# Kernel optimization log

Measured on AMD Instinct MI355X. Metric: run time of the kernel, lower is better.

The kernel has to match this reference:

```python
import jax, jax.numpy as jnp
import numpy as np

L, E, H, D, F, B, CIN, N = 12, 128, 4, 32, 512, 64, 256, 257


def setup_inputs() -> dict:
    key = jax.random.key(0)
    ks = jax.random.split(key, 10)
    s = 0.02
    rn = lambda k, shape: jax.random.normal(k, shape, jnp.float32) * s
    return {
        "feat": jax.random.normal(ks[0], (B, CIN, 32, 32), jnp.float32),
        "conv_w": rn(ks[1], (E, CIN, 3, 3)),
        "conv_b": jnp.zeros((E,), jnp.float32),
        "pos_emb": rn(ks[2], (1, N, E)),
        "cls_token": rn(ks[3], (1, 1, E)),
        "ln1_s": jnp.ones((L, E), jnp.float32),
        "ln1_b": jnp.zeros((L, E), jnp.float32),
        "qkv_w": rn(ks[4], (L, 3 * E, E)),
        "qkv_b": jnp.zeros((L, 3 * E), jnp.float32),
        "proj_w": rn(ks[5], (L, E, E)),
        "proj_b": jnp.zeros((L, E), jnp.float32),
        "ln2_s": jnp.ones((L, E), jnp.float32),
        "ln2_b": jnp.zeros((L, E), jnp.float32),
        "ffn1_w": rn(ks[6], (L, F, E)),
        "ffn1_b": jnp.zeros((L, F), jnp.float32),
        "ffn2_w": rn(ks[7], (L, E, F)),
        "ffn2_b": jnp.zeros((L, E), jnp.float32),
        "fn_s": jnp.ones((E,), jnp.float32),
        "fn_b": jnp.zeros((E,), jnp.float32),
        "fc_w": rn(ks[8], (2, E)),
        "fc_b": jnp.zeros((2,), jnp.float32),
    }


def _ln(x, s, b, eps):
    m = jnp.mean(x, -1, keepdims=True)
    v = jnp.mean((x - m) ** 2, -1, keepdims=True)
    return (x - m) * jax.lax.rsqrt(v + eps) * s + b


def reference(feat, conv_w, conv_b, pos_emb, cls_token, ln1_s, ln1_b, qkv_w,
              qkv_b, proj_w, proj_b, ln2_s, ln2_b, ffn1_w, ffn1_b, ffn2_w,
              ffn2_b, fn_s, fn_b, fc_w, fc_b):
    # patch embed: 3x3 conv stride 2 -> 16x16 = 256 tokens
    emb = jax.lax.conv_general_dilated(
        feat, conv_w, (2, 2), ((1, 1), (1, 1)),
        dimension_numbers=("NCHW", "OIHW", "NCHW")) + conv_b[None, :, None, None]
    Bsz = emb.shape[0]
    emb = emb.reshape(Bsz, E, -1).transpose(0, 2, 1)  # [B, 256, E]
    x = jnp.concatenate([jnp.broadcast_to(cls_token, (Bsz, 1, E)), emb], axis=1)
    x = x + pos_emb  # [B, N, E]
    scale = (E // H) ** -0.5

    def block(x, p):
        l1s, l1b, qw, qb, pw, pb, l2s, l2b, w1, b1, w2, b2 = p
        h = _ln(x, l1s, l1b, 1e-5)
        qkv = (h @ qw.T + qb).reshape(Bsz, N, 3, H, D).transpose(2, 0, 3, 1, 4)
        q, k, v = qkv[0], qkv[1], qkv[2]  # [B, H, N, D]
        att = jax.nn.softmax(jnp.einsum("bhnd,bhmd->bhnm", q, k) * scale, axis=-1)
        o = jnp.einsum("bhnm,bhmd->bhnd", att, v).transpose(0, 2, 1, 3).reshape(Bsz, N, E)
        x = x + (o @ pw.T + pb)
        h2 = _ln(x, l2s, l2b, 1e-5)
        x = x + (jax.nn.gelu(h2 @ w1.T + b1, approximate=False) @ w2.T + b2)
        return x, None

    x, _ = jax.lax.scan(block, x, (ln1_s, ln1_b, qkv_w, qkv_b, proj_w, proj_b,
                                   ln2_s, ln2_b, ffn1_w, ffn1_b, ffn2_w, ffn2_b))
    x = _ln(x, fn_s, fn_b, 1e-6)
    out_feat = x[:, 0, :]
    out = out_feat @ fc_w.T + fc_b
    return (out, out_feat)
```

## Files before the change

### kernel.cpp

```cpp
#include <hip/hip_runtime.h>
#include <math.h>

constexpr int NP_ = 272;
constexpr int MP_ = 64 * NP_;
constexpr int TPB_ = 17;

typedef short short8 __attribute__((ext_vector_type(8)));
typedef float f32x4 __attribute__((ext_vector_type(4)));

__device__ inline short f2bs(float f) {
    unsigned u = __builtin_bit_cast(unsigned, f);
    unsigned r = (u + 0x7fffu + ((u >> 16) & 1u)) >> 16;
    return (short)r;
}

__device__ inline f32x4 mfma16(short8 a, short8 b, f32x4 c) {
    return __builtin_amdgcn_mfma_f32_16x16x32_bf16(a, b, c, 0, 0, 0);
}

__global__ void repack_all(const float* __restrict__ qkvw, const float* __restrict__ projw,
                           const float* __restrict__ f1w, const float* __restrict__ f2w,
                           const float* __restrict__ convw,
                           short* __restrict__ wq, short* __restrict__ wp,
                           short* __restrict__ w1, short* __restrict__ w2,
                           short* __restrict__ wc) {
    int o = blockIdx.x * 256 + threadIdx.x;
    if (o < 589824) {
        int l = o / 49152, r = o % 49152;
        int chunk = r / 3072, w = r % 3072;
        int n = w >> 3, k = chunk * 8 + (w & 7);
        wq[o] = f2bs(qkvw[(size_t)l * 49152 + n * 128 + k]);
        return;
    }
    o -= 589824;
    if (o < 196608) {
        int l = o / 16384, r = o % 16384;
        int chunk = r / 1024, w = r % 1024;
        int n = w >> 3, k = chunk * 8 + (w & 7);
        wp[o] = f2bs(projw[(size_t)l * 16384 + n * 128 + k]);
        return;
    }
    o -= 196608;
    if (o < 786432) {
        int l = o / 65536, r = o % 65536;
        int chunk = r / 4096, w = r % 4096;
        int n = w >> 3, k = chunk * 8 + (w & 7);
        w1[o] = f2bs(f1w[(size_t)l * 65536 + n * 128 + k]);
        return;
    }
    o -= 786432;
    if (o < 786432) {
        int l = o / 65536, r = o % 65536;
        int chunk = r / 1024, w = r % 1024;
        int n = w >> 3, k = chunk * 8 + (w & 7);
        w2[o] = f2bs(f2w[(size_t)l * 65536 + n * 512 + k]);
        return;
    }
    o -= 786432;
    if (o < 294912) {
        int j = o & 7;
        int col = (o >> 3) & 127;
        int c = o >> 10;
        int qd = c & 3, cscb = c >> 2;
        int cs = cscb & 7, kykx = cscb >> 3;
        int cin = cs * 32 + qd * 8 + j;
        int ky = kykx / 3, kx = kykx % 3;
        wc[o] = f2bs(convw[((col * 256 + cin) * 3 + ky) * 3 + kx]);
    }
}

__global__ __launch_bounds__(256) void feat_nhwc(const float* __restrict__ feat, short* __restrict__ fp) {
    __shared__ float tile[32][33];
    int b = blockIdx.x >> 5, y = blockIdx.x & 31;
    int t = threadIdx.x;
    for (int c0 = 0; c0 < 256; c0 += 32) {
        int ci = t >> 5, x = t & 31;
        for (int cc = ci; cc < 32; cc += 8)
            tile[cc][x] = feat[((size_t)(b * 256 + c0 + cc) * 32 + y) * 32 + x];
        __syncthreads();
        for (int i = t; i < 1024; i += 256) {
            int c = i & 31, x2 = i >> 5;
            fp[((size_t)(b * 34 + y + 1) * 34 + x2 + 1) * 256 + c0 + c] = f2bs(tile[c][x2]);
        }
        __syncthreads();
    }
    short* rowp = fp + (size_t)(b * 34 + y + 1) * 34 * 256;
    for (int c = t; c < 256; c += 256) { rowp[c] = 0; rowp[33 * 256 + c] = 0; }
    if (y == 0) {
        short* r0 = fp + (size_t)(b * 34) * 34 * 256;
        for (int i = t; i < 34 * 256; i += 256) r0[i] = 0;
    }
    if (y == 31) {
        short* r33 = fp + (size_t)(b * 34 + 33) * 34 * 256;
        for (int i = t; i < 34 * 256; i += 256) r33[i] = 0;
    }
}

__global__ __launch_bounds__(256) void conv_gemm(const short* __restrict__ fp, const short* __restrict__ wr,
                                                 const float* __restrict__ cb, const float* __restrict__ pos,
                                                 const float* __restrict__ cls, float* __restrict__ X) {
    __shared__ __align__(16) short Ain[3 * 34 * 256];
    int b = blockIdx.x >> 4, oy = blockIdx.x & 15;
    int tid = threadIdx.x;
    for (int idx = tid; idx < 3 * 34 * 32; idx += 256) {
        int r = idx / 1088, rem = idx - r * 1088;
        int x = rem >> 5, c = rem & 31;
        short8 v = *(const short8*)(fp + ((size_t)(b * 34 + 2 * oy + r) * 34 + x) * 256 + c * 8);
        *(short8*)(Ain + (r * 34 + x) * 256 + ((c ^ ((x >> 1) & 7)) * 8)) = v;
    }
    __syncthreads();
    int wave = tid >> 6, lane = tid & 63;
    int ng = wave, lo = lane & 15, qd = lane >> 4;
    f32x4 acc[2] = {};
#pragma unroll
    for (int ky = 0; ky < 3; ++ky)
#pragma unroll
        for (int kx = 0; kx < 3; ++kx) {
            int sx = 2 * lo + kx;
            int arow = (ky * 34 + sx) * 256;
            int sw = (sx >> 1) & 7;
            const short* wb = wr + (((size_t)((ky * 3 + kx) * 8) * 4 + qd) * 128 + ng * 32 + lo) * 8;
#pragma unroll
            for (int cs = 0; cs < 8; ++cs) {
                short8 af = *(const short8*)(Ain + arow + (((cs * 4 + qd) ^ sw) * 8));
                short8 b0 = *(const short8*)(wb + (size_t)cs * 4096);
                short8 b1 = *(const short8*)(wb + (size_t)cs * 4096 + 128);
                acc[0] = mfma16(af, b0, acc[0]);
                acc[1] = mfma16(af, b1, acc[1]);
            }
        }
#pragma unroll
    for (int t = 0; t < 2; ++t) {
        int e = ng * 32 + t * 16 + lo;
        float bias = cb[e];
#pragma unroll
        for (int r = 0; r < 4; ++r) {
            int tok = 1 + oy * 16 + qd * 4 + r;
            X[((size_t)b * NP_ + tok) * 128 + e] = acc[t][r] + bias + pos[tok * 128 + e];
        }
    }
    if (oy == 0) {
        if (tid < 128) X[(size_t)b * NP_ * 128 + tid] = cls[tid] + pos[tid];
        for (int idx = tid; idx < 15 * 128; idx += 256)
            X[((size_t)b * NP_ + 257) * 128 + idx] = 0.f;
    }
}

__device__ inline void ln_tile16(const float* Xl, const float* __restrict__ s, const float* __restrict__ bb,
                                 short* SB, int tid, float eps) {
    int wv = tid >> 6, lane = tid & 63;
    int r4 = lane & 3, c32 = lane >> 2;
    int row = wv * 4 + r4;
    const float* xr = Xl + row * 132 + c32 * 8;
    float4 a = *(const float4*)(xr);
    float4 b = *(const float4*)(xr + 4);
    float v[8] = {a.x, a.y, a.z, a.w, b.x, b.y, b.z, b.w};
    float sum = v[0] + v[1] + v[2] + v[3] + v[4] + v[5] + v[6] + v[7];
    sum += __shfl_xor(sum, 4); sum += __shfl_xor(sum, 8);
    sum += __shfl_xor(sum, 16); sum += __shfl_xor(sum, 32);
    float mean = sum * (1.f / 128.f);
    float vs = 0.f;
#pragma unroll
    for (int j = 0; j < 8; ++j) { float d = v[j] - mean; vs += d * d; }
    vs += __shfl_xor(vs, 4); vs += __shfl_xor(vs, 8);
    vs += __shfl_xor(vs, 16); vs += __shfl_xor(vs, 32);
    float rs = rsqrtf(vs * (1.f / 128.f) + eps);
    float4 s0 = *(const float4*)(s + c32 * 8), s1 = *(const float4*)(s + c32 * 8 + 4);
    float4 b0 = *(const float4*)(bb + c32 * 8), b1 = *(const float4*)(bb + c32 * 8 + 4);
    float sv[8] = {s0.x, s0.y, s0.z, s0.w, s1.x, s1.y, s1.z, s1.w};
    float bv[8] = {b0.x, b0.y, b0.z, b0.w, b1.x, b1.y, b1.z, b1.w};
    short8 o;
#pragma unroll
    for (int j = 0; j < 8; ++j) o[j] = f2bs((v[j] - mean) * rs * sv[j] + bv[j]);
    *(short8*)(SB + (c32 * 16 + row) * 8) = o;
}

__device__ inline void qkv_stage16(const short* SB, const short* __restrict__ wq, const float* __restrict__ qb,
                                   const short8* pre, int mg, int wv, int lo, int qd,
                                   short* __restrict__ Qf, short* __restrict__ Kf, short* __restrict__ Vt) {
    int n0 = wv * 96;
    f32x4 acc[6] = {};
#pragma unroll
    for (int ki = 0; ki < 4; ++ki) {
        int kq = ki * 4 + qd;
        short8 a = *(const short8*)(SB + (kq * 16 + lo) * 8);
#pragma unroll
        for (int t = 0; t < 6; ++t) {
            short8 bf = (ki == 0) ? pre[t]
                                  : *(const short8*)(wq + ((size_t)kq * 384 + n0 + t * 16 + lo) * 8);
            acc[t] = mfma16(a, bf, acc[t]);
        }
    }
#pragma unroll
    for (int t = 0; t < 6; ++t) {
        int n = n0 + t * 16 + lo;
        float bvv = qb[n];
        int seg = n >> 7, m = n & 127, h = m >> 5, d = m & 31;
#pragma unroll
        for (int r = 0; r < 4; ++r) {
            int row = mg * 16 + qd * 4 + r;
            int bb2 = row / NP_, q = row - bb2 * NP_;
            short val = f2bs(acc[t][r] + bvv);
            if (seg == 2)
                Vt[((size_t)(bb2 * 4 + h) * 32 + d) * NP_ + q] = val;
            else
                (seg ? Kf : Qf)[((size_t)(bb2 * 4 + h) * 4 + (d >> 3)) * (NP_ * 8) + q * 8 + (d & 7)] = val;
        }
    }
}

__global__ __launch_bounds__(256, 4) void qkv0(const float* __restrict__ X, const short* __restrict__ wq,
                                               const float* __restrict__ qb, const float* __restrict__ ls,
                                               const float* __restrict__ lb,
                                               short* __restrict__ Qf, short* __restrict__ Kf,
                                               short* __restrict__ Vt) {
    __shared__ __align__(16) float Xl[16 * 132];
    __shared__ __align__(16) short SB[2048];
    int mg = blockIdx.x, tid = threadIdx.x;
    int wv = tid >> 6, lane = tid & 63, lo = lane & 15, qd = lane >> 4;
    for (int idx = tid; idx < 512; idx += 256) {
        int tok = idx >> 5, c = idx & 31;
        *(float4*)(Xl + tok * 132 + c * 4) = *(const float4*)(X + (size_t)(mg * 16 + tok) * 128 + c * 4);
    }
    short8 preq[6];
#pragma unroll
    for (int t = 0; t < 6; ++t)
        preq[t] = *(const short8*)(wq + ((size_t)qd * 384 + wv * 96 + t * 16 + lo) * 8);
    __syncthreads();
    ln_tile16(Xl, ls, lb, SB, tid, 1e-5f);
    __syncthreads();
    qkv_stage16(SB, wq, qb, preq, mg, wv, lo, qd, Qf, Kf, Vt);
}

template <int LAST>
__global__ __launch_bounds__(256, 4) void layer_tail(
    const short* __restrict__ Of, const short* __restrict__ wp, const float* __restrict__ pb,
    const float* __restrict__ l2s, const float* __restrict__ l2b,
    const short* __restrict__ w1, const float* __restrict__ b1,
    const short* __restrict__ w2, const float* __restrict__ b2,
    float* __restrict__ X,
    const float* __restrict__ l1s, const float* __restrict__ l1b,
    const short* __restrict__ wq, const float* __restrict__ qb,
    short* __restrict__ Qf, short* __restrict__ Kf, short* __restrict__ Vt) {
    __shared__ __align__(16) short SB[2048];
    __shared__ __align__(16) float Xl[16 * 132];
    __shared__ __align__(16) short Uh[32 * 136];
    int mg = blockIdx.x, tid = threadIdx.x;
    int wv = tid >> 6, lane = tid & 63, lo = lane & 15, qd = lane >> 4;
    const short* osrc = Of + (size_t)mg * 2048;
    for (int idx = tid; idx < 256; idx += 256)
        *(short8*)(SB + idx * 8) = *(const short8*)(osrc + idx * 8);
    for (int idx = tid; idx < 512; idx += 256) {
        int tok = idx >> 5, c = idx & 31;
        *(float4*)(Xl + tok * 132 + c * 4) = *(const float4*)(X + (size_t)(mg * 16 + tok) * 128 + c * 4);
    }
    int n0 = wv * 32;
    short8 prep[8];
#pragma unroll
    for (int ki = 0; ki < 4; ++ki) {
        int kq = ki * 4 + qd;
        prep[ki * 2] = *(const short8*)(wp + ((size_t)kq * 128 + n0 + lo) * 8);
        prep[ki * 2 + 1] = *(const short8*)(wp + ((size_t)kq * 128 + n0 + 16 + lo) * 8);
    }
    __syncthreads();
    {
        f32x4 pa[2] = {};
#pragma unroll
        for (int ki = 0; ki < 4; ++ki) {
            int kq = ki * 4 + qd;
            short8 a = *(const short8*)(SB + (kq * 16 + lo) * 8);
            pa[0] = mfma16(a, prep[ki * 2], pa[0]);
            pa[1] = mfma16(a, prep[ki * 2 + 1], pa[1]);
        }
        float pb0 = pb[n0 + lo], pb1 = pb[n0 + 16 + lo];
#pragma unroll
        for (int r = 0; r < 4; ++r) {
            Xl[(qd * 4 + r) * 132 + n0 + lo] += pa[0][r] + pb0;
            Xl[(qd * 4 + r) * 132 + n0 + 16 + lo] += pa[1][r] + pb1;
        }
    }
    int n0h = wv * 64;
    short8 pre1[4];
#pragma unroll
    for (int t = 0; t < 4; ++t)
        pre1[t] = *(const short8*)(w1 + ((size_t)qd * 512 + n0h + t * 16 + lo) * 8);
    __syncthreads();
    ln_tile16(Xl, l2s, l2b, SB, tid, 1e-5f);
    __syncthreads();
    f32x4 facc[2] = {};
    {
        f32x4 fa[4] = {};
#pragma unroll
        for (int ki = 0; ki < 4; ++ki) {
            int kq = ki * 4 + qd;
            short8 a = *(const short8*)(SB + (kq * 16 + lo) * 8);
#pragma unroll
            for (int t = 0; t < 4; ++t) {
                short8 bf = (ki == 0) ? pre1[t]
                                      : *(const short8*)(w1 + ((size_t)kq * 512 + n0h + t * 16 + lo) * 8);
                fa[t] = mfma16(a, bf, fa[t]);
            }
        }
#pragma unroll
        for (int t = 0; t < 4; ++t) {
            int nl = n0h + t * 16 + lo;
            float bvv = b1[nl];
#pragma unroll
            for (int r = 0; r < 4; ++r) {
                float x = fa[t][r] + bvv;
                float u = x * (0.7978845608f + 0.0356774081f * x * x);
                x = x / (1.f + __expf(-2.f * u));
                Uh[(nl >> 3) * 136 + (qd * 4 + r) * 8 + (nl & 7)] = f2bs(x);
            }
        }
    }
    short8 pre2a = *(const short8*)(w2 + ((size_t)qd * 128 + n0 + lo) * 8);
    short8 pre2b = *(const short8*)(w2 + ((size_t)qd * 128 + n0 + 16 + lo) * 8);
    short8 pre1b[4];
#pragma unroll
    for (int t = 0; t < 4; ++t)
        pre1b[t] = *(const short8*)(w1 + ((size_t)qd * 512 + 256 + n0h + t * 16 + lo) * 8);
    __syncthreads();
#pragma unroll
    for (int ki = 0; ki < 8; ++ki) {
        int kq2 = ki * 4 + qd;
        short8 a = *(const short8*)(Uh + kq2 * 136 + lo * 8);
        short8 b0 = (ki == 0) ? pre2a : *(const short8*)(w2 + ((size_t)kq2 * 128 + n0 + lo) * 8);
        short8 b1 = (ki == 0) ? pre2b : *(const short8*)(w2 + ((size_t)kq2 * 128 + n0 + 16 + lo) * 8);
        facc[0] = mfma16(a, b0, facc[0]);
        facc[1] = mfma16(a, b1, facc[1]);
    }
    short8 pre3a = *(const short8*)(w2 + ((size_t)(32 + qd) * 128 + n0 + lo) * 8);
    short8 pre3b = *(const short8*)(w2 + ((size_t)(32 + qd) * 128 + n0 + 16 + lo) * 8);
    __syncthreads();
    {
        f32x4 fa[4] = {};
#pragma unroll
        for (int ki = 0; ki < 4; ++ki) {
            int kq = ki * 4 + qd;
            short8 a = *(const short8*)(SB + (kq * 16 + lo) * 8);
#pragma unroll
            for (int t = 0; t < 4; ++t) {
                short8 bf = (ki == 0) ? pre1b[t]
                                      : *(const short8*)(w1 + ((size_t)kq * 512 + 256 + n0h + t * 16 + lo) * 8);
                fa[t] = mfma16(a, bf, fa[t]);
            }
        }
#pragma unroll
        for (int t = 0; t < 4; ++t) {
            int nl = n0h + t * 16 + lo;
            float bvv = b1[256 + nl];
#pragma unroll
            for (int r = 0; r < 4; ++r) {
                float x = fa[t][r] + bvv;
                float u = x * (0.7978845608f + 0.0356774081f * x * x);
                x = x / (1.f + __expf(-2.f * u));
                Uh[(nl >> 3) * 136 + (qd * 4 + r) * 8 + (nl & 7)] = f2bs(x);
            }
        }
    }
    __syncthreads();
#pragma unroll
    for (int ki = 0; ki < 8; ++ki) {
        int kq2 = ki * 4 + qd;
        short8 a = *(const short8*)(Uh + kq2 * 136 + lo * 8);
        short8 b0 = (ki == 0) ? pre3a : *(const short8*)(w2 + ((size_t)(32 + kq2) * 128 + n0 + lo) * 8);
        short8 b1 = (ki == 0) ? pre3b : *(const short8*)(w2 + ((size_t)(32 + kq2) * 128 + n0 + 16 + lo) * 8);
        facc[0] = mfma16(a, b0, facc[0]);
        facc[1] = mfma16(a, b1, facc[1]);
    }
    {
        float b20 = b2[n0 + lo], b21 = b2[n0 + 16 + lo];
#pragma unroll
        for (int r = 0; r < 4; ++r) {
            Xl[(qd * 4 + r) * 132 + n0 + lo] += facc[0][r] + b20;
            Xl[(qd * 4 + r) * 132 + n0 + 16 + lo] += facc[1][r] + b21;
        }
    }
    short8 preq[6];
    if (!LAST) {
#pragma unroll
        for (int t = 0; t < 6; ++t)
            preq[t] = *(const short8*)(wq + ((size_t)qd * 384 + wv * 96 + t * 16 + lo) * 8);
    }
    __syncthreads();
    for (int idx = tid; idx < 512; idx += 256) {
        int tok = idx >> 5, c = idx & 31;
        *(float4*)(X + (size_t)(mg * 16 + tok) * 128 + c * 4) = *(const float4*)(Xl + tok * 132 + c * 4);
    }
    if (LAST) return;
    ln_tile16(Xl, l1s, l1b, SB, tid, 1e-5f);
    __syncthreads();
    qkv_stage16(SB, wq, qb, preq, mg, wv, lo, qd, Qf, Kf, Vt);
}

__global__ __launch_bounds__(256, 4) void attn(const short* __restrict__ Qf, const short* __restrict__ Kf,
                                               const short* __restrict__ Vt, short* __restrict__ Of) {
    __shared__ __align__(16) short Vl[32 * 296];
    __shared__ __align__(16) short Pl[4][544];
    int b = blockIdx.x >> 4, h = (blockIdx.x >> 2) & 3, qc = blockIdx.x & 3;
    int tid = threadIdx.x;
    const short* kf = Kf + (size_t)(b * 4 + h) * (4 * NP_ * 8);
    const short* qf = Qf + (size_t)(b * 4 + h) * (4 * NP_ * 8);
    const short* vt = Vt + (size_t)(b * 4 + h) * (32 * NP_);
    for (int idx = tid; idx < 32 * 37; idx += 256) {
        int d = idx / 37, c8 = idx - d * 37;
        short8 v = {};
        if (c8 < 34) v = *(const short8*)(vt + d * NP_ + c8 * 8);
        *(short8*)(Vl + d * 296 + c8 * 8) = v;
    }
    __syncthreads();
    int wv = tid >> 6, lane = tid & 63, lo = lane & 15, qd = lane >> 4;
    short* Pw = Pl[wv];
    const float scale = 0.17677669529663687f;
    for (int it = 0; it < 2; ++it) {
        int qt;
        if (it == 0) qt = qc * 4 + wv;
        else { if ((qc | wv) != 0) break; qt = 16; }
        short8 qfr = *(const short8*)(qf + ((size_t)qd * NP_ + qt * 16 + lo) * 8);
        f32x4 sc[17];
#pragma unroll
        for (int kt = 0; kt < 17; ++kt) {
            short8 kfr = *(const short8*)(kf + ((size_t)qd * NP_ + kt * 16 + lo) * 8);
            f32x4 z = {};
            sc[kt] = mfma16(qfr, kfr, z);
        }
        float mx[4] = {-1e30f, -1e30f, -1e30f, -1e30f};
#pragma unroll
        for (int kt = 0; kt < 17; ++kt) {
            bool valid = (kt * 16 + lo) < 257;
#pragma unroll
            for (int r = 0; r < 4; ++r) {
                float v2 = valid ? sc[kt][r] * scale : -1e30f;
                sc[kt][r] = v2;
                mx[r] = fmaxf(mx[r], v2);
            }
        }
#pragma unroll
        for (int r = 0; r < 4; ++r) {
            mx[r] = fmaxf(mx[r], __shfl_xor(mx[r], 1));
            mx[r] = fmaxf(mx[r], __shfl_xor(mx[r], 2));
            mx[r] = fmaxf(mx[r], __shfl_xor(mx[r], 4));
            mx[r] = fmaxf(mx[r], __shfl_xor(mx[r], 8));
        }
        float l[4] = {0.f, 0.f, 0.f, 0.f};
#pragma unroll
        for (int kt = 0; kt < 17; ++kt)
#pragma unroll
            for (int r = 0; r < 4; ++r) {
                float p = __expf(sc[kt][r] - mx[r]);
                sc[kt][r] = p;
                l[r] += p;
            }
#pragma unroll
        for (int r = 0; r < 4; ++r) {
            l[r] += __shfl_xor(l[r], 1);
            l[r] += __shfl_xor(l[r], 2);
            l[r] += __shfl_xor(l[r], 4);
            l[r] += __shfl_xor(l[r], 8);
        }
        float rl[4];
#pragma unroll
        for (int r = 0; r < 4; ++r) rl[r] = 1.f / l[r];
        f32x4 oa[2] = {};
#pragma unroll
        for (int ks = 0; ks < 9; ++ks) {
#pragma unroll
            for (int kt2 = 0; kt2 < 2; ++kt2) {
                int kt = ks * 2 + kt2;
                int lkey = kt2 * 16 + lo;
#pragma unroll
                for (int r = 0; r < 4; ++r) {
                    short pv = (kt < 17) ? f2bs(sc[kt][r] * rl[r]) : (short)0;
                    Pw[(lkey >> 3) * 128 + (qd * 4 + r) * 8 + (lkey & 7)] = pv;
                }
            }
            short8 pf = *(const short8*)(Pw + (qd * 16 + lo) * 8);
#pragma unroll
            for (int nt = 0; nt < 2; ++nt) {
                short8 vfr = *(const short8*)(Vl + (nt * 16 + lo) * 296 + ks * 32 + qd * 8);
                oa[nt] = mfma16(pf, vfr, oa[nt]);
            }
        }
        int tile = b * TPB_ + qt;
#pragma unroll
        for (int nt = 0; nt < 2; ++nt)
#pragma unroll
            for (int r = 0; r < 4; ++r) {
                int qq = qt * 16 + qd * 4 + r;
                if (qq <= 256) {
                    int col = h * 32 + nt * 16 + lo;
                    Of[(size_t)tile * 2048 + (col >> 3) * 128 + (qd * 4 + r) * 8 + (col & 7)] = f2bs(oa[nt][r]);
                }
            }
    }
}

__global__ __launch_bounds__(64) void final_head(const float* __restrict__ X, const float* __restrict__ fs,
                                                 const float* __restrict__ fb, const float* __restrict__ fcw,
                                                 const float* __restrict__ fcb, float* __restrict__ out) {
    int b = blockIdx.x, lane = threadIdx.x;
    float2 v = *(const float2*)(X + (size_t)b * NP_ * 128 + lane * 2);
    float sum = v.x + v.y;
#pragma unroll
    for (int m = 1; m < 64; m <<= 1) sum += __shfl_xor(sum, m);
    float mean = sum * (1.f / 128.f);
    float d0 = v.x - mean, d1 = v.y - mean;
    float vs = d0 * d0 + d1 * d1;
#pragma unroll
    for (int m = 1; m < 64; m <<= 1) vs += __shfl_xor(vs, m);
    float rs = rsqrtf(vs * (1.f / 128.f) + 1e-6f);
    int e = lane * 2;
    float f0 = d0 * rs * fs[e] + fb[e];
    float f1 = d1 * rs * fs[e + 1] + fb[e + 1];
    out[128 + b * 128 + e] = f0;
    out[128 + b * 128 + e + 1] = f1;
    float p0 = f0 * fcw[e] + f1 * fcw[e + 1];
    float p1 = f0 * fcw[128 + e] + f1 * fcw[128 + e + 1];
#pragma unroll
    for (int m = 1; m < 64; m <<= 1) {
        p0 += __shfl_xor(p0, m);
        p1 += __shfl_xor(p1, m);
    }
    if (lane == 0) {
        out[b * 2 + 0] = p0 + fcb[0];
        out[b * 2 + 1] = p1 + fcb[1];
    }
}

extern "C" void kernel_launch(void* const* d_in, const int* in_sizes, int n_in,
                              void* d_out, int out_size, void* d_ws, size_t ws_size,
                              hipStream_t stream) {
    const float* feat    = (const float*)d_in[0];
    const float* conv_w  = (const float*)d_in[1];
    const float* conv_b  = (const float*)d_in[2];
    const float* pos_emb = (const float*)d_in[3];
    const float* cls_tok = (const float*)d_in[4];
    const float* ln1_s   = (const float*)d_in[5];
    const float* ln1_b   = (const float*)d_in[6];
    const float* qkv_w   = (const float*)d_in[7];
    const float* qkv_b   = (const float*)d_in[8];
    const float* proj_w  = (const float*)d_in[9];
    const float* proj_b  = (const float*)d_in[10];
    const float* ln2_s   = (const float*)d_in[11];
    const float* ln2_b   = (const float*)d_in[12];
    const float* ffn1_w  = (const float*)d_in[13];
    const float* ffn1_b  = (const float*)d_in[14];
    const float* ffn2_w  = (const float*)d_in[15];
    const float* ffn2_b  = (const float*)d_in[16];
    const float* fn_s    = (const float*)d_in[17];
    const float* fn_b    = (const float*)d_in[18];
    const float* fc_w    = (const float*)d_in[19];
    const float* fc_b    = (const float*)d_in[20];

    char* p = (char*)d_ws;
    auto alloc = [&](size_t bytes) { char* r = p; p += (bytes + 255) & ~(size_t)255; return r; };
    short* wq  = (short*)alloc((size_t)589824 * 2);
    short* wp  = (short*)alloc((size_t)196608 * 2);
    short* w1  = (short*)alloc((size_t)786432 * 2);
    short* w2  = (short*)alloc((size_t)786432 * 2);
    short* wc  = (short*)alloc((size_t)294912 * 2);
    short* fpd = (short*)alloc((size_t)64 * 34 * 34 * 256 * 2);
    float* X   = (float*)alloc((size_t)MP_ * 128 * 4);
    short* Qf  = (short*)alloc((size_t)64 * 16 * NP_ * 8 * 2);
    short* Kf  = (short*)alloc((size_t)64 * 16 * NP_ * 8 * 2);
    short* Vt  = (short*)alloc((size_t)64 * 4 * 32 * NP_ * 2);
    short* Of  = (short*)alloc((size_t)(MP_ / 16) * 2048 * 2);

    repack_all<<<10368, 256, 0, stream>>>(qkv_w, proj_w, ffn1_w, ffn2_w, conv_w, wq, wp, w1, w2, wc);
    feat_nhwc<<<64 * 32, 256, 0, stream>>>(feat, fpd);
    conv_gemm<<<1024, 256, 0, stream>>>(fpd, wc, conv_b, pos_emb, cls_tok, X);

    qkv0<<<1088, 256, 0, stream>>>(X, wq, qkv_b, ln1_s, ln1_b, Qf, Kf, Vt);
    for (int l = 0; l < 12; ++l) {
        attn<<<1024, 256, 0, stream>>>(Qf, Kf, Vt, Of);
        if (l < 11)
            layer_tail<0><<<1088, 256, 0, stream>>>(Of, wp + (size_t)l * 16384, proj_b + l * 128,
                                                    ln2_s + l * 128, ln2_b + l * 128,
                                                    w1 + (size_t)l * 65536, ffn1_b + l * 512,
                                                    w2 + (size_t)l * 65536, ffn2_b + l * 128, X,
                                                    ln1_s + (l + 1) * 128, ln1_b + (l + 1) * 128,
                                                    wq + (size_t)(l + 1) * 49152, qkv_b + (l + 1) * 384,
                                                    Qf, Kf, Vt);
        else
            layer_tail<1><<<1088, 256, 0, stream>>>(Of, wp + (size_t)l * 16384, proj_b + l * 128,
                                                    ln2_s + l * 128, ln2_b + l * 128,
                                                    w1 + (size_t)l * 65536, ffn1_b + l * 512,
                                                    w2 + (size_t)l * 65536, ffn2_b + l * 128, X,
                                                    ln1_s, ln1_b, wq, qkv_b, Qf, Kf, Vt);
    }
    final_head<<<64, 64, 0, stream>>>(X, fn_s, fn_b, fc_w, fc_b, (float*)d_out);
}
```

Baseline: 807.8 us.

## Process 32-row tiles in layer kernels and fuse NHWC repack into conv

The per-layer tail and QKV kernels now handle 32 token rows per block instead of 16. Each weight fragment loaded from global memory feeds two MFMA row tiles, which halves weight traffic per token, and the grid shrinks from 1088 to 544 blocks. Separately, the feat_nhwc pass and its padded bf16 buffer are removed: conv_gemm now reads fp32 NCHW input directly, converts it to bf16, and handles the zero padding in shared memory. The cost is more registers and LDS per block, so occupancy is lowered to 3 blocks, and each block does strided scalar LDS writes during the conv load.

```diff
diff --git a/kernel.cpp b/kernel.cpp
--- a/kernel.cpp
+++ b/kernel.cpp
@@ -69,44 +69,35 @@
     }
 }
 
-__global__ __launch_bounds__(256) void feat_nhwc(const float* __restrict__ feat, short* __restrict__ fp) {
-    __shared__ float tile[32][33];
-    int b = blockIdx.x >> 5, y = blockIdx.x & 31;
-    int t = threadIdx.x;
-    for (int c0 = 0; c0 < 256; c0 += 32) {
-        int ci = t >> 5, x = t & 31;
-        for (int cc = ci; cc < 32; cc += 8)
-            tile[cc][x] = feat[((size_t)(b * 256 + c0 + cc) * 32 + y) * 32 + x];
-        __syncthreads();
-        for (int i = t; i < 1024; i += 256) {
-            int c = i & 31, x2 = i >> 5;
-            fp[((size_t)(b * 34 + y + 1) * 34 + x2 + 1) * 256 + c0 + c] = f2bs(tile[c][x2]);
-        }
-        __syncthreads();
-    }
-    short* rowp = fp + (size_t)(b * 34 + y + 1) * 34 * 256;
-    for (int c = t; c < 256; c += 256) { rowp[c] = 0; rowp[33 * 256 + c] = 0; }
-    if (y == 0) {
-        short* r0 = fp + (size_t)(b * 34) * 34 * 256;
-        for (int i = t; i < 34 * 256; i += 256) r0[i] = 0;
-    }
-    if (y == 31) {
-        short* r33 = fp + (size_t)(b * 34 + 33) * 34 * 256;
-        for (int i = t; i < 34 * 256; i += 256) r33[i] = 0;
-    }
-}
-
-__global__ __launch_bounds__(256) void conv_gemm(const short* __restrict__ fp, const short* __restrict__ wr,
+__global__ __launch_bounds__(256) void conv_gemm(const float* __restrict__ feat, const short* __restrict__ wr,
                                                  const float* __restrict__ cb, const float* __restrict__ pos,
                                                  const float* __restrict__ cls, float* __restrict__ X) {
     __shared__ __align__(16) short Ain[3 * 34 * 256];
     int b = blockIdx.x >> 4, oy = blockIdx.x & 15;
     int tid = threadIdx.x;
-    for (int idx = tid; idx < 3 * 34 * 32; idx += 256) {
-        int r = idx / 1088, rem = idx - r * 1088;
-        int x = rem >> 5, c = rem & 31;
-        short8 v = *(const short8*)(fp + ((size_t)(b * 34 + 2 * oy + r) * 34 + x) * 256 + c * 8);
-        *(short8*)(Ain + (r * 34 + x) * 256 + ((c ^ ((x >> 1) & 7)) * 8)) = v;
+    for (int idx = tid; idx < 6144; idx += 256) {
+        int x4 = idx & 7;
+        int cin = (idx >> 3) & 255;
+        int r = idx >> 11;
+        int y = 2 * oy + r - 1;
+        float4 f = make_float4(0.f, 0.f, 0.f, 0.f);
+        if (y >= 0 && y < 32)
+            f = *(const float4*)(feat + (((size_t)(b * 256 + cin) * 32 + y) * 32 + x4 * 4));
+        int cg = cin >> 3, c7 = cin & 7;
+        float vv[4] = {f.x, f.y, f.z, f.w};
+#pragma unroll
+        for (int dx = 0; dx < 4; ++dx) {
+            int px = x4 * 4 + 1 + dx;
+            int sw = (px >> 1) & 7;
+            Ain[(r * 34 + px) * 256 + ((cg ^ sw) * 8) + c7] = f2bs(vv[dx]);
+        }
+    }
+    for (int idx = tid; idx < 1536; idx += 256) {
+        int c = idx & 255;
+        int j = idx >> 8;
+        int r = j >> 1;
+        int px = (j & 1) ? 33 : 0;
+        Ain[(r * 34 + px) * 256 + c] = 0;
     }
     __syncthreads();
     int wave = tid >> 6, lane = tid & 63;
@@ -175,52 +166,56 @@
     *(short8*)(SB + (c32 * 16 + row) * 8) = o;
 }
 
-__device__ inline void qkv_stage16(const short* SB, const short* __restrict__ wq, const float* __restrict__ qb,
+__device__ inline void qkv_stage32(const short* SB, const short* __restrict__ wq, const float* __restrict__ qb,
                                    const short8* pre, int mg, int wv, int lo, int qd,
                                    short* __restrict__ Qf, short* __restrict__ Kf, short* __restrict__ Vt) {
     int n0 = wv * 96;
-    f32x4 acc[6] = {};
+    f32x4 acc[2][6] = {};
 #pragma unroll
     for (int ki = 0; ki < 4; ++ki) {
         int kq = ki * 4 + qd;
-        short8 a = *(const short8*)(SB + (kq * 16 + lo) * 8);
+        short8 a0 = *(const short8*)(SB + (kq * 16 + lo) * 8);
+        short8 a1 = *(const short8*)(SB + 2048 + (kq * 16 + lo) * 8);
 #pragma unroll
         for (int t = 0; t < 6; ++t) {
             short8 bf = (ki == 0) ? pre[t]
                                   : *(const short8*)(wq + ((size_t)kq * 384 + n0 + t * 16 + lo) * 8);
-            acc[t] = mfma16(a, bf, acc[t]);
-        }
-    }
-#pragma unroll
-    for (int t = 0; t < 6; ++t) {
-        int n = n0 + t * 16 + lo;
-        float bvv = qb[n];
-        int seg = n >> 7, m = n & 127, h = m >> 5, d = m & 31;
-#pragma unroll
-        for (int r = 0; r < 4; ++r) {
-            int row = mg * 16 + qd * 4 + r;
-            int bb2 = row / NP_, q = row - bb2 * NP_;
-            short val = f2bs(acc[t][r] + bvv);
-            if (seg == 2)
-                Vt[((size_t)(bb2 * 4 + h) * 32 + d) * NP_ + q] = val;
-            else
-                (seg ? Kf : Qf)[((size_t)(bb2 * 4 + h) * 4 + (d >> 3)) * (NP_ * 8) + q * 8 + (d & 7)] = val;
-        }
-    }
-}
-
-__global__ __launch_bounds__(256, 4) void qkv0(const float* __restrict__ X, const short* __restrict__ wq,
+            acc[0][t] = mfma16(a0, bf, acc[0][t]);
+            acc[1][t] = mfma16(a1, bf, acc[1][t]);
+        }
+    }
+#pragma unroll
+    for (int mt = 0; mt < 2; ++mt)
+#pragma unroll
+        for (int t = 0; t < 6; ++t) {
+            int n = n0 + t * 16 + lo;
+            float bvv = qb[n];
+            int seg = n >> 7, m = n & 127, h = m >> 5, d = m & 31;
+#pragma unroll
+            for (int r = 0; r < 4; ++r) {
+                int row = mg * 32 + mt * 16 + qd * 4 + r;
+                int bb2 = row / NP_, q = row - bb2 * NP_;
+                short val = f2bs(acc[mt][t][r] + bvv);
+                if (seg == 2)
+                    Vt[((size_t)(bb2 * 4 + h) * 32 + d) * NP_ + q] = val;
+                else
+                    (seg ? Kf : Qf)[((size_t)(bb2 * 4 + h) * 4 + (d >> 3)) * (NP_ * 8) + q * 8 + (d & 7)] = val;
+            }
+        }
+}
+
+__global__ __launch_bounds__(256, 3) void qkv0(const float* __restrict__ X, const short* __restrict__ wq,
                                                const float* __restrict__ qb, const float* __restrict__ ls,
                                                const float* __restrict__ lb,
                                                short* __restrict__ Qf, short* __restrict__ Kf,
                                                short* __restrict__ Vt) {
-    __shared__ __align__(16) float Xl[16 * 132];
-    __shared__ __align__(16) short SB[2048];
+    __shared__ __align__(16) float Xl[32 * 132];
+    __shared__ __align__(16) short SB[2 * 2048];
     int mg = blockIdx.x, tid = threadIdx.x;
     int wv = tid >> 6, lane = tid & 63, lo = lane & 15, qd = lane >> 4;
-    for (int idx = tid; idx < 512; idx += 256) {
+    for (int idx = tid; idx < 1024; idx += 256) {
         int tok = idx >> 5, c = idx & 31;
-        *(float4*)(Xl + tok * 132 + c * 4) = *(const float4*)(X + (size_t)(mg * 16 + tok) * 128 + c * 4);
+        *(float4*)(Xl + tok * 132 + c * 4) = *(const float4*)(X + (size_t)(mg * 32 + tok) * 128 + c * 4);
     }
     short8 preq[6];
 #pragma unroll
@@ -228,12 +223,13 @@
         preq[t] = *(const short8*)(wq + ((size_t)qd * 384 + wv * 96 + t * 16 + lo) * 8);
     __syncthreads();
     ln_tile16(Xl, ls, lb, SB, tid, 1e-5f);
-    __syncthreads();
-    qkv_stage16(SB, wq, qb, preq, mg, wv, lo, qd, Qf, Kf, Vt);
+    ln_tile16(Xl + 16 * 132, ls, lb, SB + 2048, tid, 1e-5f);
+    __syncthreads();
+    qkv_stage32(SB, wq, qb, preq, mg, wv, lo, qd, Qf, Kf, Vt);
 }
 
 template <int LAST>
-__global__ __launch_bounds__(256, 4) void layer_tail(
+__global__ __launch_bounds__(256, 3) void layer_tail(
     const short* __restrict__ Of, const short* __restrict__ wp, const float* __restrict__ pb,
     const float* __restrict__ l2s, const float* __restrict__ l2b,
     const short* __restrict__ w1, const float* __restrict__ b1,
@@ -242,17 +238,17 @@
     const float* __restrict__ l1s, const float* __restrict__ l1b,
     const short* __restrict__ wq, const float* __restrict__ qb,
     short* __restrict__ Qf, short* __restrict__ Kf, short* __restrict__ Vt) {
-    __shared__ __align__(16) short SB[2048];
-    __shared__ __align__(16) float Xl[16 * 132];
-    __shared__ __align__(16) short Uh[32 * 136];
+    __shared__ __align__(16) short SB[2 * 2048];
+    __shared__ __align__(16) float Xl[32 * 132];
+    __shared__ __align__(16) short Uh[2 * 32 * 136];
     int mg = blockIdx.x, tid = threadIdx.x;
     int wv = tid >> 6, lane = tid & 63, lo = lane & 15, qd = lane >> 4;
-    const short* osrc = Of + (size_t)mg * 2048;
-    for (int idx = tid; idx < 256; idx += 256)
+    const short* osrc = Of + (size_t)mg * 4096;
+    for (int idx = tid; idx < 512; idx += 256)
         *(short8*)(SB + idx * 8) = *(const short8*)(osrc + idx * 8);
-    for (int idx = tid; idx < 512; idx += 256) {
+    for (int idx = tid; idx < 1024; idx += 256) {
         int tok = idx >> 5, c = idx & 31;
-        *(float4*)(Xl + tok * 132 + c * 4) = *(const float4*)(X + (size_t)(mg * 16 + tok) * 128 + c * 4);
+        *(float4*)(Xl + tok * 132 + c * 4) = *(const float4*)(X + (size_t)(mg * 32 + tok) * 128 + c * 4);
     }
     int n0 = wv * 32;
     short8 prep[8];
@@ -264,20 +260,25 @@
     }
     __syncthreads();
     {
-        f32x4 pa[2] = {};
+        f32x4 pa[2][2] = {};
 #pragma unroll
         for (int ki = 0; ki < 4; ++ki) {
             int kq = ki * 4 + qd;
-            short8 a = *(const short8*)(SB + (kq * 16 + lo) * 8);
-            pa[0] = mfma16(a, prep[ki * 2], pa[0]);
-            pa[1] = mfma16(a, prep[ki * 2 + 1], pa[1]);
+            short8 a0 = *(const short8*)(SB + (kq * 16 + lo) * 8);
+            short8 a1 = *(const short8*)(SB + 2048 + (kq * 16 + lo) * 8);
+            pa[0][0] = mfma16(a0, prep[ki * 2], pa[0][0]);
+            pa[0][1] = mfma16(a0, prep[ki * 2 + 1], pa[0][1]);
+            pa[1][0] = mfma16(a1, prep[ki * 2], pa[1][0]);
+            pa[1][1] = mfma16(a1, prep[ki * 2 + 1], pa[1][1]);
         }
         float pb0 = pb[n0 + lo], pb1 = pb[n0 + 16 + lo];
 #pragma unroll
-        for (int r = 0; r < 4; ++r) {
-            Xl[(qd * 4 + r) * 132 + n0 + lo] += pa[0][r] + pb0;
-            Xl[(qd * 4 + r) * 132 + n0 + 16 + lo] += pa[1][r] + pb1;
-        }
+        for (int mt = 0; mt < 2; ++mt)
+#pragma unroll
+            for (int r = 0; r < 4; ++r) {
+                Xl[(mt * 16 + qd * 4 + r) * 132 + n0 + lo] += pa[mt][0][r] + pb0;
+                Xl[(mt * 16 + qd * 4 + r) * 132 + n0 + 16 + lo] += pa[mt][1][r] + pb1;
+            }
     }
     int n0h = wv * 64;
     short8 pre1[4];
@@ -286,19 +287,22 @@
         pre1[t] = *(const short8*)(w1 + ((size_t)qd * 512 + n0h + t * 16 + lo) * 8);
     __syncthreads();
     ln_tile16(Xl, l2s, l2b, SB, tid, 1e-5f);
-    __syncthreads();
-    f32x4 facc[2] = {};
+    ln_tile16(Xl + 16 * 132, l2s, l2b, SB + 2048, tid, 1e-5f);
+    __syncthreads();
+    f32x4 facc[2][2] = {};
     {
-        f32x4 fa[4] = {};
+        f32x4 fa[2][4] = {};
 #pragma unroll
         for (int ki = 0; ki < 4; ++ki) {
             int kq = ki * 4 + qd;
-            short8 a = *(const short8*)(SB + (kq * 16 + lo) * 8);
+            short8 a0 = *(const short8*)(SB + (kq * 16 + lo) * 8);
+            short8 a1 = *(const short8*)(SB + 2048 + (kq * 16 + lo) * 8);
 #pragma unroll
             for (int t = 0; t < 4; ++t) {
                 short8 bf = (ki == 0) ? pre1[t]
                                       : *(const short8*)(w1 + ((size_t)kq * 512 + n0h + t * 16 + lo) * 8);
-                fa[t] = mfma16(a, bf, fa[t]);
+                fa[0][t] = mfma16(a0, bf, fa[0][t]);
+                fa[1][t] = mfma16(a1, bf, fa[1][t]);
             }
         }
 #pragma unroll
@@ -306,12 +310,14 @@
             int nl = n0h + t * 16 + lo;
             float bvv = b1[nl];
 #pragma unroll
-            for (int r = 0; r < 4; ++r) {
-                float x = fa[t][r] + bvv;
-                float u = x * (0.7978845608f + 0.0356774081f * x * x);
-                x = x / (1.f + __expf(-2.f * u));
-                Uh[(nl >> 3) * 136 + (qd * 4 + r) * 8 + (nl & 7)] = f2bs(x);
-            }
+            for (int mt = 0; mt < 2; ++mt)
+#pragma unroll
+                for (int r = 0; r < 4; ++r) {
+                    float x = fa[mt][t][r] + bvv;
+                    float u = x * (0.7978845608f + 0.0356774081f * x * x);
+                    x = x / (1.f + __expf(-2.f * u));
+                    Uh[(mt * 32 + (nl >> 3)) * 136 + (qd * 4 + r) * 8 + (nl & 7)] = f2bs(x);
+                }
         }
     }
     short8 pre2a = *(const short8*)(w2 + ((size_t)qd * 128 + n0 + lo) * 8);
@@ -324,26 +330,31 @@
 #pragma unroll
     for (int ki = 0; ki < 8; ++ki) {
         int kq2 = ki * 4 + qd;
-        short8 a = *(const short8*)(Uh + kq2 * 136 + lo * 8);
+        short8 a0 = *(const short8*)(Uh + kq2 * 136 + lo * 8);
+        short8 a1 = *(const short8*)(Uh + (32 + kq2) * 136 + lo * 8);
         short8 b0 = (ki == 0) ? pre2a : *(const short8*)(w2 + ((size_t)kq2 * 128 + n0 + lo) * 8);
         short8 b1 = (ki == 0) ? pre2b : *(const short8*)(w2 + ((size_t)kq2 * 128 + n0 + 16 + lo) * 8);
-        facc[0] = mfma16(a, b0, facc[0]);
-        facc[1] = mfma16(a, b1, facc[1]);
+        facc[0][0] = mfma16(a0, b0, facc[0][0]);
+        facc[0][1] = mfma16(a0, b1, facc[0][1]);
+        facc[1][0] = mfma16(a1, b0, facc[1][0]);
+        facc[1][1] = mfma16(a1, b1, facc[1][1]);
     }
     short8 pre3a = *(const short8*)(w2 + ((size_t)(32 + qd) * 128 + n0 + lo) * 8);
     short8 pre3b = *(const short8*)(w2 + ((size_t)(32 + qd) * 128 + n0 + 16 + lo) * 8);
     __syncthreads();
     {
-        f32x4 fa[4] = {};
+        f32x4 fa[2][4] = {};
 #pragma unroll
         for (int ki = 0; ki < 4; ++ki) {
             int kq = ki * 4 + qd;
-            short8 a = *(const short8*)(SB + (kq * 16 + lo) * 8);
+            short8 a0 = *(const short8*)(SB + (kq * 16 + lo) * 8);
+            short8 a1 = *(const short8*)(SB + 2048 + (kq * 16 + lo) * 8);
 #pragma unroll
             for (int t = 0; t < 4; ++t) {
                 short8 bf = (ki == 0) ? pre1b[t]
                                       : *(const short8*)(w1 + ((size_t)kq * 512 + 256 + n0h + t * 16 + lo) * 8);
-                fa[t] = mfma16(a, bf, fa[t]);
+                fa[0][t] = mfma16(a0, bf, fa[0][t]);
+                fa[1][t] = mfma16(a1, bf, fa[1][t]);
             }
         }
 #pragma unroll
@@ -351,31 +362,38 @@
             int nl = n0h + t * 16 + lo;
             float bvv = b1[256 + nl];
 #pragma unroll
-            for (int r = 0; r < 4; ++r) {
-                float x = fa[t][r] + bvv;
-                float u = x * (0.7978845608f + 0.0356774081f * x * x);
-                x = x / (1.f + __expf(-2.f * u));
-                Uh[(nl >> 3) * 136 + (qd * 4 + r) * 8 + (nl & 7)] = f2bs(x);
-            }
+            for (int mt = 0; mt < 2; ++mt)
+#pragma unroll
+                for (int r = 0; r < 4; ++r) {
+                    float x = fa[mt][t][r] + bvv;
+                    float u = x * (0.7978845608f + 0.0356774081f * x * x);
+                    x = x / (1.f + __expf(-2.f * u));
+                    Uh[(mt * 32 + (nl >> 3)) * 136 + (qd * 4 + r) * 8 + (nl & 7)] = f2bs(x);
+                }
         }
     }
     __syncthreads();
 #pragma unroll
     for (int ki = 0; ki < 8; ++ki) {
         int kq2 = ki * 4 + qd;
-        short8 a = *(const short8*)(Uh + kq2 * 136 + lo * 8);
+        short8 a0 = *(const short8*)(Uh + kq2 * 136 + lo * 8);
+        short8 a1 = *(const short8*)(Uh + (32 + kq2) * 136 + lo * 8);
         short8 b0 = (ki == 0) ? pre3a : *(const short8*)(w2 + ((size_t)(32 + kq2) * 128 + n0 + lo) * 8);
         short8 b1 = (ki == 0) ? pre3b : *(const short8*)(w2 + ((size_t)(32 + kq2) * 128 + n0 + 16 + lo) * 8);
-        facc[0] = mfma16(a, b0, facc[0]);
-        facc[1] = mfma16(a, b1, facc[1]);
+        facc[0][0] = mfma16(a0, b0, facc[0][0]);
+        facc[0][1] = mfma16(a0, b1, facc[0][1]);
+        facc[1][0] = mfma16(a1, b0, facc[1][0]);
+        facc[1][1] = mfma16(a1, b1, facc[1][1]);
     }
     {
         float b20 = b2[n0 + lo], b21 = b2[n0 + 16 + lo];
 #pragma unroll
-        for (int r = 0; r < 4; ++r) {
-            Xl[(qd * 4 + r) * 132 + n0 + lo] += facc[0][r] + b20;
-            Xl[(qd * 4 + r) * 132 + n0 + 16 + lo] += facc[1][r] + b21;
-        }
+        for (int mt = 0; mt < 2; ++mt)
+#pragma unroll
+            for (int r = 0; r < 4; ++r) {
+                Xl[(mt * 16 + qd * 4 + r) * 132 + n0 + lo] += facc[mt][0][r] + b20;
+                Xl[(mt * 16 + qd * 4 + r) * 132 + n0 + 16 + lo] += facc[mt][1][r] + b21;
+            }
     }
     short8 preq[6];
     if (!LAST) {
@@ -384,14 +402,15 @@
             preq[t] = *(const short8*)(wq + ((size_t)qd * 384 + wv * 96 + t * 16 + lo) * 8);
     }
     __syncthreads();
-    for (int idx = tid; idx < 512; idx += 256) {
+    for (int idx = tid; idx < 1024; idx += 256) {
         int tok = idx >> 5, c = idx & 31;
-        *(float4*)(X + (size_t)(mg * 16 + tok) * 128 + c * 4) = *(const float4*)(Xl + tok * 132 + c * 4);
+        *(float4*)(X + (size_t)(mg * 32 + tok) * 128 + c * 4) = *(const float4*)(Xl + tok * 132 + c * 4);
     }
     if (LAST) return;
     ln_tile16(Xl, l1s, l1b, SB, tid, 1e-5f);
-    __syncthreads();
-    qkv_stage16(SB, wq, qb, preq, mg, wv, lo, qd, Qf, Kf, Vt);
+    ln_tile16(Xl + 16 * 132, l1s, l1b, SB + 2048, tid, 1e-5f);
+    __syncthreads();
+    qkv_stage32(SB, wq, qb, preq, mg, wv, lo, qd, Qf, Kf, Vt);
 }
 
 __global__ __launch_bounds__(256, 4) void attn(const short* __restrict__ Qf, const short* __restrict__ Kf,
@@ -560,7 +579,6 @@
     short* w1  = (short*)alloc((size_t)786432 * 2);
     short* w2  = (short*)alloc((size_t)786432 * 2);
     short* wc  = (short*)alloc((size_t)294912 * 2);
-    short* fpd = (short*)alloc((size_t)64 * 34 * 34 * 256 * 2);
     float* X   = (float*)alloc((size_t)MP_ * 128 * 4);
     short* Qf  = (short*)alloc((size_t)64 * 16 * NP_ * 8 * 2);
     short* Kf  = (short*)alloc((size_t)64 * 16 * NP_ * 8 * 2);
@@ -568,26 +586,25 @@
     short* Of  = (short*)alloc((size_t)(MP_ / 16) * 2048 * 2);
 
     repack_all<<<10368, 256, 0, stream>>>(qkv_w, proj_w, ffn1_w, ffn2_w, conv_w, wq, wp, w1, w2, wc);
-    feat_nhwc<<<64 * 32, 256, 0, stream>>>(feat, fpd);
-    conv_gemm<<<1024, 256, 0, stream>>>(fpd, wc, conv_b, pos_emb, cls_tok, X);
-
-    qkv0<<<1088, 256, 0, stream>>>(X, wq, qkv_b, ln1_s, ln1_b, Qf, Kf, Vt);
+    conv_gemm<<<1024, 256, 0, stream>>>(feat, wc, conv_b, pos_emb, cls_tok, X);
+
+    qkv0<<<544, 256, 0, stream>>>(X, wq, qkv_b, ln1_s, ln1_b, Qf, Kf, Vt);
     for (int l = 0; l < 12; ++l) {
         attn<<<1024, 256, 0, stream>>>(Qf, Kf, Vt, Of);
         if (l < 11)
-            layer_tail<0><<<1088, 256, 0, stream>>>(Of, wp + (size_t)l * 16384, proj_b + l * 128,
-                                                    ln2_s + l * 128, ln2_b + l * 128,
-                                                    w1 + (size_t)l * 65536, ffn1_b + l * 512,
-                                                    w2 + (size_t)l * 65536, ffn2_b + l * 128, X,
-                                                    ln1_s + (l + 1) * 128, ln1_b + (l + 1) * 128,
-                                                    wq + (size_t)(l + 1) * 49152, qkv_b + (l + 1) * 384,
-                                                    Qf, Kf, Vt);
+            layer_tail<0><<<544, 256, 0, stream>>>(Of, wp + (size_t)l * 16384, proj_b + l * 128,
+                                                   ln2_s + l * 128, ln2_b + l * 128,
+                                                   w1 + (size_t)l * 65536, ffn1_b + l * 512,
+                                                   w2 + (size_t)l * 65536, ffn2_b + l * 128, X,
+                                                   ln1_s + (l + 1) * 128, ln1_b + (l + 1) * 128,
+                                                   wq + (size_t)(l + 1) * 49152, qkv_b + (l + 1) * 384,
+                                                   Qf, Kf, Vt);
         else
-            layer_tail<1><<<1088, 256, 0, stream>>>(Of, wp + (size_t)l * 16384, proj_b + l * 128,
-                                                    ln2_s + l * 128, ln2_b + l * 128,
-                                                    w1 + (size_t)l * 65536, ffn1_b + l * 512,
-                                                    w2 + (size_t)l * 65536, ffn2_b + l * 128, X,
-                                                    ln1_s, ln1_b, wq, qkv_b, Qf, Kf, Vt);
+            layer_tail<1><<<544, 256, 0, stream>>>(Of, wp + (size_t)l * 16384, proj_b + l * 128,
+                                                   ln2_s + l * 128, ln2_b + l * 128,
+                                                   w1 + (size_t)l * 65536, ffn1_b + l * 512,
+                                                   w2 + (size_t)l * 65536, ffn2_b + l * 128, X,
+                                                   ln1_s, ln1_b, wq, qkv_b, Qf, Kf, Vt);
     }
     final_head<<<64, 64, 0, stream>>>(X, fn_s, fn_b, fc_w, fc_b, (float*)d_out);
 }
```

Measured after the change: 782.2 us. 3.2% less time.
